# Optimization experiments

Hardware: AMD Instinct MI355X
Metric: run time of the kernel (lower is better)

The kernel has to match this reference:

```python
import jax, jax.numpy as jnp
import numpy as np

N_NODES = 50000
D_MODEL = 128
N_EDGES = 600000
HIDDEN = 128
EDGE_FEAT = 2 * D_MODEL + 2  # 258


def setup_inputs() -> dict:
    key = jax.random.key(0)
    k = jax.random.split(key, 8)
    H = jax.random.normal(k[0], (N_NODES, D_MODEL), dtype=jnp.float32)
    edge_index = jax.random.randint(k[1], (2, N_EDGES), 0, N_NODES, dtype=jnp.int64)
    S_e = jax.random.uniform(k[2], (N_EDGES,), dtype=jnp.float32)
    F_e = jax.random.uniform(k[3], (N_EDGES,), dtype=jnp.float32)
    W1 = jax.random.normal(k[4], (EDGE_FEAT, HIDDEN), dtype=jnp.float32) * (1.0 / np.sqrt(EDGE_FEAT))
    b1 = jnp.zeros((HIDDEN,), dtype=jnp.float32)
    W2 = jax.random.normal(k[5], (HIDDEN, 1), dtype=jnp.float32) * (1.0 / np.sqrt(HIDDEN))
    b2 = jnp.zeros((1,), dtype=jnp.float32)
    return {"H": H, "edge_index": edge_index, "S_e": S_e, "F_e": F_e,
            "W1": W1, "b1": b1, "W2": W2, "b2": b2}


def reference(H, edge_index, S_e, F_e, W1, b1, W2, b2):
    # Gather endpoint node features: [E, D]
    H_u = H[edge_index[0]]
    H_v = H[edge_index[1]]
    H_diff = jnp.abs(H_u - H_v)
    H_prod = H_u * H_v
    # [E, 2D+2]
    edge_features = jnp.concatenate(
        [H_diff, H_prod, S_e[:, None], F_e[:, None]], axis=1)
    # 2-layer MLP with SiLU (dropout is identity in eval mode)
    h = jax.nn.silu(edge_features @ W1 + b1)
    a_e = (h @ W2 + b2)[:, 0]  # [E]
    return a_e
```

## Files before the change

### kernel.cpp

```cpp
#include <hip/hip_runtime.h>


typedef _Float16       half8   __attribute__((ext_vector_type(8)));
typedef _Float16       half4v  __attribute__((ext_vector_type(4)));
typedef unsigned short ushort8 __attribute__((ext_vector_type(8)));
typedef float          f32x4   __attribute__((ext_vector_type(4)));

#define NSEG       8
#define W1T_STRIDE 288

__device__ __forceinline__ float silu_f(float x) {
    return x / (1.0f + __expf(-x));
}

__device__ __forceinline__ void canon(int u, int v, int& a, int& b) {
    const int sw = (u ^ v) & 1;
    a = sw ? v : u;
    b = sw ? u : v;
}


__global__ __launch_bounds__(256)
void cvt_hist_kernel(const float* __restrict__ H, _Float16* __restrict__ Hh,
                     int n4, const int* __restrict__ eidx,
                     int* __restrict__ hist, int E, int ASZ, int BBINS) {
    int i = blockIdx.x * blockDim.x + threadIdx.x;
    if (i < n4) {
        const float4 f = ((const float4*)H)[i];
        half4v h;
        h[0] = (_Float16)f.x; h[1] = (_Float16)f.y;
        h[2] = (_Float16)f.z; h[3] = (_Float16)f.w;
        ((half4v*)Hh)[i] = h;
    }
    if (i < E) {
        int a, b;
        canon(eidx[i], eidx[E + i], a, b);
        atomicAdd(&hist[(a / ASZ) * BBINS + (b >> 3)], 1);
    }
}

__global__ __launch_bounds__(256)
void scan_kernel(int* __restrict__ hist, int* __restrict__ bsum,
                 int NB, int nb1, int* __restrict__ flag,
                 int* __restrict__ vbs, int BBINS, int E) {
    __shared__ int s[256];
    __shared__ int lastBlk;
    const int t = threadIdx.x;
    const int i = blockIdx.x * 256 + t;
    const int v = (i < NB) ? hist[i] : 0;
    s[t] = v;
    __syncthreads();
    for (int off = 1; off < 256; off <<= 1) {
        const int x = (t >= off) ? s[t - off] : 0;
        __syncthreads();
        s[t] += x;
        __syncthreads();
    }
    if (i < NB) hist[i] = s[t] - v;
    if (t == 255) bsum[blockIdx.x] = s[255];
    __threadfence();
    if (t == 0) lastBlk = (atomicAdd(flag, 1) == (int)gridDim.x - 1);
    __syncthreads();
    if (!lastBlk) return;
    const int bv = (t < nb1) ? atomicAdd(&bsum[t], 0) : 0;
    s[t] = bv;
    __syncthreads();
    for (int off = 1; off < 256; off <<= 1) {
        const int x = (t >= off) ? s[t - off] : 0;
        __syncthreads();
        s[t] += x;
        __syncthreads();
    }
    if (t < nb1) bsum[t] = s[t] - bv;
    __syncthreads();
    if (t < NSEG) {
        const int idx = t * BBINS;
        vbs[t] = atomicAdd(&hist[idx], 0) + bsum[idx >> 8];
    } else if (t == NSEG) {
        vbs[NSEG] = E;
    }
}

__global__ __launch_bounds__(256)
void scatter_kernel(const int* __restrict__ eidx, const float* __restrict__ Se,
                    const float* __restrict__ Fe, int* __restrict__ ofs,
                    const int* __restrict__ bsum,
                    int4* __restrict__ recs, int E, int ASZ, int BBINS) {
    int e = blockIdx.x * blockDim.x + threadIdx.x;
    if (e < E) {
        int a, b;
        canon(eidx[e], eidx[E + e], a, b);
        const int key = (a / ASZ) * BBINS + (b >> 3);
        const int pos = atomicAdd(&ofs[key], 1) + bsum[key >> 8];
        _Float16 sh = (_Float16)Se[e];
        _Float16 fh = (_Float16)Fe[e];
        unsigned pk = (unsigned)*(unsigned short*)&sh
                    | ((unsigned)*(unsigned short*)&fh << 16);
        recs[pos] = make_int4(a, b, e, (int)pk);
    }
}


__device__ __forceinline__ void stage_w1(const float* __restrict__ W1,
                                         const float* __restrict__ b1,
                                         _Float16* __restrict__ w1t, int tid) {
    const int n = tid & 127;
    const int g = tid >> 7;
    #pragma unroll
    for (int i = 0; i < 9; ++i) {
        const int kb = g + (i << 2);
        half8 tmp;
        if (kb < 32) {
            #pragma unroll
            for (int j = 0; j < 8; ++j) {
                const int kp  = (kb << 3) + j;
                const int c   = kp >> 5;
                const int k32 = kp & 31;
                const int src = ((c & 1) << 7) + ((c >> 1) << 5) + k32;
                tmp[j] = (_Float16)W1[src * 128 + n];
            }
            *(half8*)&w1t[n * W1T_STRIDE + ((kb ^ (n & 7)) << 3)] = tmp;
        } else {
            const int k32b = (kb - 32) << 3;
            #pragma unroll
            for (int j = 0; j < 8; ++j) {
                const int k32 = k32b + j;
                float v = 0.f;
                if (k32 == 0)      v = W1[32768 + n];
                else if (k32 == 1) v = W1[32896 + n];
                else if (k32 == 2) v = b1[n];
                tmp[j] = (_Float16)v;
            }
            *(half8*)&w1t[n * W1T_STRIDE + (kb << 3)] = tmp;
        }
    }
}


__device__ __forceinline__ void edge_tile32(
    const _Float16* __restrict__ Hh, const int4* __restrict__ recs,
    const _Float16* __restrict__ w1t,
    const f32x4* __restrict__ w2r, float b2v, float* __restrict__ out,
    int ebase, int elim, int q, int cb, int swz)
{
    const int eA = min(ebase + cb, elim - 1);
    const int eB = min(ebase + 16 + cb, elim - 1);
    const int4 rA = recs[eA];
    const int4 rB = recs[eB];

    const _Float16* upA = Hh + (size_t)rA.x * 128;
    const _Float16* vpA = Hh + (size_t)rA.y * 128;
    const _Float16* upB = Hh + (size_t)rB.x * 128;
    const _Float16* vpB = Hh + (size_t)rB.y * 128;

    f32x4 accA[8], accB[8];
    #pragma unroll
    for (int t = 0; t < 8; ++t) {
        accA[t] = (f32x4){0.f, 0.f, 0.f, 0.f};
        accB[t] = (f32x4){0.f, 0.f, 0.f, 0.f};
    }

    #pragma unroll
    for (int c8 = 0; c8 < 4; ++c8) {
        const half8 u8A = *(const half8*)(upA + (c8 << 5) + (q << 3));
        const half8 v8A = *(const half8*)(vpA + (c8 << 5) + (q << 3));
        const half8 u8B = *(const half8*)(upB + (c8 << 5) + (q << 3));
        const half8 v8B = *(const half8*)(vpB + (c8 << 5) + (q << 3));
        half8 dA = u8A - v8A;
        half8 dB = u8B - v8B;
        ushort8 duA = *(ushort8*)&dA; duA = duA & (unsigned short)0x7FFF;
        ushort8 duB = *(ushort8*)&dB; duB = duB & (unsigned short)0x7FFF;
        const half8 aeA = *(half8*)&duA;
        const half8 aeB = *(half8*)&duB;
        const half8 aoA = u8A * v8A;
        const half8 aoB = u8B * v8B;

        const int kb0 = ((c8 << 3) + q) ^ swz;
        const int kb1 = ((c8 << 3) + 4 + q) ^ swz;
        #pragma unroll
        for (int t = 0; t < 8; ++t) {
            const half8 b0 = *(const half8*)&w1t[((t << 4) + cb) * W1T_STRIDE + (kb0 << 3)];
            accA[t] = __builtin_amdgcn_mfma_f32_16x16x32_f16(b0, aeA, accA[t], 0, 0, 0);
            accB[t] = __builtin_amdgcn_mfma_f32_16x16x32_f16(b0, aeB, accB[t], 0, 0, 0);
        }
        #pragma unroll
        for (int t = 0; t < 8; ++t) {
            const half8 b1f = *(const half8*)&w1t[((t << 4) + cb) * W1T_STRIDE + (kb1 << 3)];
            accA[t] = __builtin_amdgcn_mfma_f32_16x16x32_f16(b1f, aoA, accA[t], 0, 0, 0);
            accB[t] = __builtin_amdgcn_mfma_f32_16x16x32_f16(b1f, aoB, accB[t], 0, 0, 0);
        }
    }

    half8 aEA, aEB;
    #pragma unroll
    for (int j = 0; j < 8; ++j) { aEA[j] = (_Float16)0.f; aEB[j] = (_Float16)0.f; }
    if (q == 0) {
        const unsigned short slA = (unsigned short)((unsigned)rA.w & 0xFFFF);
        const unsigned short flA = (unsigned short)((unsigned)rA.w >> 16);
        const unsigned short slB = (unsigned short)((unsigned)rB.w & 0xFFFF);
        const unsigned short flB = (unsigned short)((unsigned)rB.w >> 16);
        aEA[0] = *(const _Float16*)&slA;
        aEA[1] = *(const _Float16*)&flA;
        aEA[2] = (_Float16)1.0f;
        aEB[0] = *(const _Float16*)&slB;
        aEB[1] = *(const _Float16*)&flB;
        aEB[2] = (_Float16)1.0f;
    }
    #pragma unroll
    for (int t = 0; t < 8; ++t) {
        const half8 bE = *(const half8*)&w1t[((t << 4) + cb) * W1T_STRIDE + ((32 + q) << 3)];
        accA[t] = __builtin_amdgcn_mfma_f32_16x16x32_f16(bE, aEA, accA[t], 0, 0, 0);
        accB[t] = __builtin_amdgcn_mfma_f32_16x16x32_f16(bE, aEB, accB[t], 0, 0, 0);
    }

    float rsA = 0.f, rsB = 0.f;
    #pragma unroll
    for (int t = 0; t < 8; ++t) {
        const f32x4 avA = accA[t];
        const f32x4 avB = accB[t];
        const f32x4 wv  = w2r[t];
        #pragma unroll
        for (int rr = 0; rr < 4; ++rr) {
            rsA += silu_f(avA[rr]) * wv[rr];
            rsB += silu_f(avB[rr]) * wv[rr];
        }
    }
    rsA += __shfl_xor(rsA, 16);
    rsA += __shfl_xor(rsA, 32);
    rsB += __shfl_xor(rsB, 16);
    rsB += __shfl_xor(rsB, 32);

    if (q == 0) {
        if (ebase + cb < elim)      out[rA.z] = rsA + b2v;
        if (ebase + 16 + cb < elim) out[rB.z] = rsB + b2v;
    }
}


__global__ __launch_bounds__(512, 2)
void edgegate_seg(const _Float16* __restrict__ Hh,
                  const int4*  __restrict__ recs,
                  const int*   __restrict__ vbs,
                  int*         __restrict__ ctr,
                  const float* __restrict__ W1,
                  const float* __restrict__ b1,
                  const float* __restrict__ W2,
                  const float* __restrict__ b2,
                  float*       __restrict__ out)
{
    __shared__ _Float16 w1t[128 * W1T_STRIDE];
    __shared__ int tkt[2];
    const int tid = threadIdx.x;
    stage_w1(W1, b1, w1t, tid);

    int xcd;
    asm volatile("s_getreg_b32 %0, hwreg(HW_REG_XCC_ID)" : "=s"(xcd));
    xcd &= (NSEG - 1);

    const int lane = tid & 63;
    const int wave = tid >> 6;
    const int q    = lane >> 4;
    const int cb   = lane & 15;
    const int swz  = cb & 7;
    const float b2v = b2[0];
    f32x4 w2r[8];
    #pragma unroll
    for (int t = 0; t < 8; ++t)
        w2r[t] = *(const f32x4*)&W2[(t << 4) + (q << 2)];

    int p = 0;
    for (int sidx = 0; sidx < NSEG; ++sidx) {
        const int seg = (xcd + sidx) & (NSEG - 1);
        const int vs  = vbs[seg];
        const int ve  = vbs[seg + 1];
        const int ner = ve - vs;
        if (ner <= 0) continue;
        const int Tt = (ner + 255) >> 8;

        __syncthreads();
        if (tid == 0) tkt[p] = atomicAdd(&ctr[seg], 1);
        __syncthreads();
        int t0 = tkt[p];
        while (t0 < Tt) {
            const int pn = p ^ 1;
            if (tid == 0) tkt[pn] = atomicAdd(&ctr[seg], 1);
            const int ebase = vs + (t0 << 8) + (wave << 5);
            edge_tile32(Hh, recs, w1t, w2r, b2v, out, ebase, ve, q, cb, swz);
            __syncthreads();
            p = pn;
            t0 = tkt[p];
        }
    }
}


__global__ __launch_bounds__(512, 2)
void edgegate_fb(const float* __restrict__ H,
                 const _Float16* __restrict__ Hh,
                 const int*   __restrict__ eidx,
                 const float* __restrict__ Se,
                 const float* __restrict__ Fe,
                 const float* __restrict__ W1,
                 const float* __restrict__ b1,
                 const float* __restrict__ W2,
                 const float* __restrict__ b2,
                 float*       __restrict__ out,
                 int E, int ntiles, int useF16)
{
    __shared__ _Float16 w1t[128 * W1T_STRIDE];
    const int tid = threadIdx.x;
    stage_w1(W1, b1, w1t, tid);

    const int lane = tid & 63;
    const int wave = tid >> 6;
    const int q    = lane >> 4;
    const int cb   = lane & 15;
    const int swz  = cb & 7;
    const float b2v = b2[0];
    f32x4 w2r[8];
    #pragma unroll
    for (int t = 0; t < 8; ++t)
        w2r[t] = *(const f32x4*)&W2[(t << 4) + (q << 2)];

    __syncthreads();

    for (int tile = blockIdx.x; tile < ntiles; tile += gridDim.x) {
        const int ebase = tile * 128 + wave * 16;
        int e = ebase + cb;
        if (e >= E) e = E - 1;
        const int u = eidx[e];
        const int v = eidx[E + e];
        const float sfe = Se[e];
        const float ffe = Fe[e];

        f32x4 acc[8];
        #pragma unroll
        for (int t = 0; t < 8; ++t) acc[t] = (f32x4){0.f, 0.f, 0.f, 0.f};

        #pragma unroll
        for (int c8 = 0; c8 < 4; ++c8) {
            half8 ae, ao;
            if (useF16) {
                const _Float16* up = Hh + (size_t)u * 128;
                const _Float16* vp = Hh + (size_t)v * 128;
                const half8 u8 = *(const half8*)(up + (c8 << 5) + (q << 3));
                const half8 v8 = *(const half8*)(vp + (c8 << 5) + (q << 3));
                half8 d8 = u8 - v8;
                ushort8 du = *(ushort8*)&d8;
                du = du & (unsigned short)0x7FFF;
                ae = *(half8*)&du;
                ao = u8 * v8;
            } else {
                const float* up = H + (size_t)u * 128;
                const float* vp = H + (size_t)v * 128;
                #pragma unroll
                for (int j = 0; j < 8; ++j) {
                    const float uu = up[(c8 << 5) + (q << 3) + j];
                    const float vv = vp[(c8 << 5) + (q << 3) + j];
                    ae[j] = (_Float16)fabsf(uu - vv);
                    ao[j] = (_Float16)(uu * vv);
                }
            }
            const int kb0 = ((c8 << 3) + q) ^ swz;
            const int kb1 = ((c8 << 3) + 4 + q) ^ swz;
            #pragma unroll
            for (int t = 0; t < 8; ++t) {
                const half8 b0 = *(const half8*)&w1t[((t << 4) + cb) * W1T_STRIDE + (kb0 << 3)];
                acc[t] = __builtin_amdgcn_mfma_f32_16x16x32_f16(b0, ae, acc[t], 0, 0, 0);
            }
            #pragma unroll
            for (int t = 0; t < 8; ++t) {
                const half8 b1f = *(const half8*)&w1t[((t << 4) + cb) * W1T_STRIDE + (kb1 << 3)];
                acc[t] = __builtin_amdgcn_mfma_f32_16x16x32_f16(b1f, ao, acc[t], 0, 0, 0);
            }
        }

        half8 aE;
        #pragma unroll
        for (int j = 0; j < 8; ++j) aE[j] = (_Float16)0.f;
        if (q == 0) {
            aE[0] = (_Float16)sfe;
            aE[1] = (_Float16)ffe;
            aE[2] = (_Float16)1.0f;
        }
        #pragma unroll
        for (int t = 0; t < 8; ++t) {
            const half8 bE = *(const half8*)&w1t[((t << 4) + cb) * W1T_STRIDE + ((32 + q) << 3)];
            acc[t] = __builtin_amdgcn_mfma_f32_16x16x32_f16(bE, aE, acc[t], 0, 0, 0);
        }

        float rs = 0.f;
        #pragma unroll
        for (int t = 0; t < 8; ++t) {
            const f32x4 av = acc[t];
            const f32x4 wv = w2r[t];
            #pragma unroll
            for (int rr = 0; rr < 4; ++rr)
                rs += silu_f(av[rr]) * wv[rr];
        }
        rs += __shfl_xor(rs, 16);
        rs += __shfl_xor(rs, 32);

        if (q == 0 && ebase + cb < E) out[ebase + cb] = rs + b2v;
    }
}


static inline size_t align256(size_t x) { return (x + 255) & ~(size_t)255; }

extern "C" void kernel_launch(void* const* d_in, const int* in_sizes, int n_in,
                              void* d_out, int out_size, void* d_ws, size_t ws_size,
                              hipStream_t stream)
{
    const float* H    = (const float*)d_in[0];
    const int*   eidx = (const int*)  d_in[1];
    const float* Se   = (const float*)d_in[2];
    const float* Fe   = (const float*)d_in[3];
    const float* W1   = (const float*)d_in[4];
    const float* b1   = (const float*)d_in[5];
    const float* W2   = (const float*)d_in[6];
    const float* b2   = (const float*)d_in[7];
    float* out = (float*)d_out;

    const int nH     = in_sizes[0];
    const int nNodes = nH / 128;
    const int E      = in_sizes[2];
    const int n4     = nH / 4;
    const int ntiles = (E + 127) / 128;

    const int ASZ   = (nNodes + NSEG - 1) / NSEG;
    const int BBINS = (nNodes + 7) >> 3;
    const int NB    = NSEG * BBINS;
    const int nb1   = (NB + 255) / 256;

    const size_t hhB    = (size_t)nH * sizeof(_Float16);
    const size_t off_g  = align256(hhB);
    const size_t off_bs = align256(off_g + (size_t)(NB + 16) * 4);
    const size_t off_vb = align256(off_bs + 256 * 4);
    const size_t off_r  = align256(off_vb + 16 * 4);
    const size_t need   = off_r + (size_t)E * sizeof(int4);

    if (ws_size >= need && nb1 <= 256) {
        _Float16* Hh   = (_Float16*)((char*)d_ws);
        int*      hist = (int*)     ((char*)d_ws + off_g);
        int*      ctr  = hist + NB;
        int*      flag = hist + NB + 8;
        int*      bsum = (int*)     ((char*)d_ws + off_bs);
        int*      vbs  = (int*)     ((char*)d_ws + off_vb);
        int4*     recs = (int4*)    ((char*)d_ws + off_r);

        const int ncvh = (n4 > E) ? n4 : E;
        hipMemsetAsync(hist, 0, (size_t)(NB + 16) * sizeof(int), stream);
        hipLaunchKernelGGL(cvt_hist_kernel, dim3((ncvh + 255) / 256), dim3(256),
                           0, stream, H, Hh, n4, eidx, hist, E, ASZ, BBINS);
        hipLaunchKernelGGL(scan_kernel, dim3(nb1), dim3(256), 0, stream,
                           hist, bsum, NB, nb1, flag, vbs, BBINS, E);
        hipLaunchKernelGGL(scatter_kernel, dim3((E + 255) / 256), dim3(256),
                           0, stream, eidx, Se, Fe, hist, bsum, recs,
                           E, ASZ, BBINS);
        hipLaunchKernelGGL(edgegate_seg, dim3(512), dim3(512), 0, stream,
                           Hh, recs, vbs, ctr, W1, b1, W2, b2, out);
    } else if (ws_size >= hhB) {
        _Float16* Hh = (_Float16*)d_ws;
        const int grid = (512 < ntiles) ? 512 : ntiles;
        hipLaunchKernelGGL(cvt_hist_kernel, dim3((n4 + 255) / 256), dim3(256),
                           0, stream, H, Hh, n4, eidx, (int*)nullptr, 0, 1, 1);
        hipLaunchKernelGGL(edgegate_fb, dim3(grid), dim3(512), 0, stream,
                           H, Hh, eidx, Se, Fe, W1, b1, W2, b2, out, E, ntiles, 1);
    } else {
        const int grid = (512 < ntiles) ? 512 : ntiles;
        hipLaunchKernelGGL(edgegate_fb, dim3(grid), dim3(512), 0, stream,
                           H, (const _Float16*)nullptr, eidx, Se, Fe, W1, b1, W2, b2,
                           out, E, ntiles, 0);
    }
}
```

Measured before the change: 299.3 us.

## Split hidden dimension across wave pairs to halve per-wave accumulators

Each tile of 32 edges is now handled by a pair of waves, and each wave computes half of the 128 hidden units, so it holds 4 accumulator tiles per edge group instead of 8. A block now processes 128 edges per ticket instead of 256. Partial second-layer sums are exchanged through shared memory, using a double-buffered slot indexed by the ticket parity, and combined after the existing barrier. The aim is to cut register pressure and per-wave latency, possibly raising occupancy. In exchange, every edge's node features are gathered twice (once per wave of the pair), twice as many tickets are taken, and an extra shared-memory combine is added.

Measured after the change: 305.7 us. 2.1% more time.

```diff
diff --git a/kernel.cpp b/kernel.cpp
--- a/kernel.cpp
+++ b/kernel.cpp
@@ -137,106 +137,6 @@
 }
 
 
-__device__ __forceinline__ void edge_tile32(
-    const _Float16* __restrict__ Hh, const int4* __restrict__ recs,
-    const _Float16* __restrict__ w1t,
-    const f32x4* __restrict__ w2r, float b2v, float* __restrict__ out,
-    int ebase, int elim, int q, int cb, int swz)
-{
-    const int eA = min(ebase + cb, elim - 1);
-    const int eB = min(ebase + 16 + cb, elim - 1);
-    const int4 rA = recs[eA];
-    const int4 rB = recs[eB];
-
-    const _Float16* upA = Hh + (size_t)rA.x * 128;
-    const _Float16* vpA = Hh + (size_t)rA.y * 128;
-    const _Float16* upB = Hh + (size_t)rB.x * 128;
-    const _Float16* vpB = Hh + (size_t)rB.y * 128;
-
-    f32x4 accA[8], accB[8];
-    #pragma unroll
-    for (int t = 0; t < 8; ++t) {
-        accA[t] = (f32x4){0.f, 0.f, 0.f, 0.f};
-        accB[t] = (f32x4){0.f, 0.f, 0.f, 0.f};
-    }
-
-    #pragma unroll
-    for (int c8 = 0; c8 < 4; ++c8) {
-        const half8 u8A = *(const half8*)(upA + (c8 << 5) + (q << 3));
-        const half8 v8A = *(const half8*)(vpA + (c8 << 5) + (q << 3));
-        const half8 u8B = *(const half8*)(upB + (c8 << 5) + (q << 3));
-        const half8 v8B = *(const half8*)(vpB + (c8 << 5) + (q << 3));
-        half8 dA = u8A - v8A;
-        half8 dB = u8B - v8B;
-        ushort8 duA = *(ushort8*)&dA; duA = duA & (unsigned short)0x7FFF;
-        ushort8 duB = *(ushort8*)&dB; duB = duB & (unsigned short)0x7FFF;
-        const half8 aeA = *(half8*)&duA;
-        const half8 aeB = *(half8*)&duB;
-        const half8 aoA = u8A * v8A;
-        const half8 aoB = u8B * v8B;
-
-        const int kb0 = ((c8 << 3) + q) ^ swz;
-        const int kb1 = ((c8 << 3) + 4 + q) ^ swz;
-        #pragma unroll
-        for (int t = 0; t < 8; ++t) {
-            const half8 b0 = *(const half8*)&w1t[((t << 4) + cb) * W1T_STRIDE + (kb0 << 3)];
-            accA[t] = __builtin_amdgcn_mfma_f32_16x16x32_f16(b0, aeA, accA[t], 0, 0, 0);
-            accB[t] = __builtin_amdgcn_mfma_f32_16x16x32_f16(b0, aeB, accB[t], 0, 0, 0);
-        }
-        #pragma unroll
-        for (int t = 0; t < 8; ++t) {
-            const half8 b1f = *(const half8*)&w1t[((t << 4) + cb) * W1T_STRIDE + (kb1 << 3)];
-            accA[t] = __builtin_amdgcn_mfma_f32_16x16x32_f16(b1f, aoA, accA[t], 0, 0, 0);
-            accB[t] = __builtin_amdgcn_mfma_f32_16x16x32_f16(b1f, aoB, accB[t], 0, 0, 0);
-        }
-    }
-
-    half8 aEA, aEB;
-    #pragma unroll
-    for (int j = 0; j < 8; ++j) { aEA[j] = (_Float16)0.f; aEB[j] = (_Float16)0.f; }
-    if (q == 0) {
-        const unsigned short slA = (unsigned short)((unsigned)rA.w & 0xFFFF);
-        const unsigned short flA = (unsigned short)((unsigned)rA.w >> 16);
-        const unsigned short slB = (unsigned short)((unsigned)rB.w & 0xFFFF);
-        const unsigned short flB = (unsigned short)((unsigned)rB.w >> 16);
-        aEA[0] = *(const _Float16*)&slA;
-        aEA[1] = *(const _Float16*)&flA;
-        aEA[2] = (_Float16)1.0f;
-        aEB[0] = *(const _Float16*)&slB;
-        aEB[1] = *(const _Float16*)&flB;
-        aEB[2] = (_Float16)1.0f;
-    }
-    #pragma unroll
-    for (int t = 0; t < 8; ++t) {
-        const half8 bE = *(const half8*)&w1t[((t << 4) + cb) * W1T_STRIDE + ((32 + q) << 3)];
-        accA[t] = __builtin_amdgcn_mfma_f32_16x16x32_f16(bE, aEA, accA[t], 0, 0, 0);
-        accB[t] = __builtin_amdgcn_mfma_f32_16x16x32_f16(bE, aEB, accB[t], 0, 0, 0);
-    }
-
-    float rsA = 0.f, rsB = 0.f;
-    #pragma unroll
-    for (int t = 0; t < 8; ++t) {
-        const f32x4 avA = accA[t];
-        const f32x4 avB = accB[t];
-        const f32x4 wv  = w2r[t];
-        #pragma unroll
-        for (int rr = 0; rr < 4; ++rr) {
-            rsA += silu_f(avA[rr]) * wv[rr];
-            rsB += silu_f(avB[rr]) * wv[rr];
-        }
-    }
-    rsA += __shfl_xor(rsA, 16);
-    rsA += __shfl_xor(rsA, 32);
-    rsB += __shfl_xor(rsB, 16);
-    rsB += __shfl_xor(rsB, 32);
-
-    if (q == 0) {
-        if (ebase + cb < elim)      out[rA.z] = rsA + b2v;
-        if (ebase + 16 + cb < elim) out[rB.z] = rsB + b2v;
-    }
-}
-
-
 __global__ __launch_bounds__(512, 2)
 void edgegate_seg(const _Float16* __restrict__ Hh,
                   const int4*  __restrict__ recs,
@@ -249,6 +149,7 @@
                   float*       __restrict__ out)
 {
     __shared__ _Float16 w1t[128 * W1T_STRIDE];
+    __shared__ float pcomb[2][4][2][16];
     __shared__ int tkt[2];
     const int tid = threadIdx.x;
     stage_w1(W1, b1, w1t, tid);
@@ -259,14 +160,16 @@
 
     const int lane = tid & 63;
     const int wave = tid >> 6;
+    const int pr   = wave >> 1;
+    const int h    = wave & 1;
     const int q    = lane >> 4;
     const int cb   = lane & 15;
     const int swz  = cb & 7;
     const float b2v = b2[0];
-    f32x4 w2r[8];
+    f32x4 w2r[4];
     #pragma unroll
-    for (int t = 0; t < 8; ++t)
-        w2r[t] = *(const f32x4*)&W2[(t << 4) + (q << 2)];
+    for (int tt = 0; tt < 4; ++tt)
+        w2r[tt] = *(const f32x4*)&W2[(((h << 2) + tt) << 4) + (q << 2)];
 
     int p = 0;
     for (int sidx = 0; sidx < NSEG; ++sidx) {
@@ -275,7 +178,7 @@
         const int ve  = vbs[seg + 1];
         const int ner = ve - vs;
         if (ner <= 0) continue;
-        const int Tt = (ner + 255) >> 8;
+        const int Tt = (ner + 127) >> 7;
 
         __syncthreads();
         if (tid == 0) tkt[p] = atomicAdd(&ctr[seg], 1);
@@ -284,9 +187,109 @@
         while (t0 < Tt) {
             const int pn = p ^ 1;
             if (tid == 0) tkt[pn] = atomicAdd(&ctr[seg], 1);
-            const int ebase = vs + (t0 << 8) + (wave << 5);
-            edge_tile32(Hh, recs, w1t, w2r, b2v, out, ebase, ve, q, cb, swz);
+
+            const int ebase = vs + (t0 << 7) + (pr << 5);
+            const int eA = min(ebase + cb, ve - 1);
+            const int eB = min(ebase + 16 + cb, ve - 1);
+            const int4 rA = recs[eA];
+            const int4 rB = recs[eB];
+
+            const _Float16* upA = Hh + (size_t)rA.x * 128;
+            const _Float16* vpA = Hh + (size_t)rA.y * 128;
+            const _Float16* upB = Hh + (size_t)rB.x * 128;
+            const _Float16* vpB = Hh + (size_t)rB.y * 128;
+
+            f32x4 accA[4], accB[4];
+            #pragma unroll
+            for (int tt = 0; tt < 4; ++tt) {
+                accA[tt] = (f32x4){0.f, 0.f, 0.f, 0.f};
+                accB[tt] = (f32x4){0.f, 0.f, 0.f, 0.f};
+            }
+
+            #pragma unroll
+            for (int c8 = 0; c8 < 4; ++c8) {
+                const half8 u8A = *(const half8*)(upA + (c8 << 5) + (q << 3));
+                const half8 v8A = *(const half8*)(vpA + (c8 << 5) + (q << 3));
+                const half8 u8B = *(const half8*)(upB + (c8 << 5) + (q << 3));
+                const half8 v8B = *(const half8*)(vpB + (c8 << 5) + (q << 3));
+                half8 dA = u8A - v8A;
+                half8 dB = u8B - v8B;
+                ushort8 duA = *(ushort8*)&dA; duA = duA & (unsigned short)0x7FFF;
+                ushort8 duB = *(ushort8*)&dB; duB = duB & (unsigned short)0x7FFF;
+                const half8 aeA = *(half8*)&duA;
+                const half8 aeB = *(half8*)&duB;
+                const half8 aoA = u8A * v8A;
+                const half8 aoB = u8B * v8B;
+
+                const int kb0 = ((c8 << 3) + q) ^ swz;
+                const int kb1 = ((c8 << 3) + 4 + q) ^ swz;
+                #pragma unroll
+                for (int tt = 0; tt < 4; ++tt) {
+                    const int row = (((h << 2) + tt) << 4) + cb;
+                    const half8 b0 = *(const half8*)&w1t[row * W1T_STRIDE + (kb0 << 3)];
+                    accA[tt] = __builtin_amdgcn_mfma_f32_16x16x32_f16(b0, aeA, accA[tt], 0, 0, 0);
+                    accB[tt] = __builtin_amdgcn_mfma_f32_16x16x32_f16(b0, aeB, accB[tt], 0, 0, 0);
+                }
+                #pragma unroll
+                for (int tt = 0; tt < 4; ++tt) {
+                    const int row = (((h << 2) + tt) << 4) + cb;
+                    const half8 b1f = *(const half8*)&w1t[row * W1T_STRIDE + (kb1 << 3)];
+                    accA[tt] = __builtin_amdgcn_mfma_f32_16x16x32_f16(b1f, aoA, accA[tt], 0, 0, 0);
+                    accB[tt] = __builtin_amdgcn_mfma_f32_16x16x32_f16(b1f, aoB, accB[tt], 0, 0, 0);
+                }
+            }
+
+            half8 aEA, aEB;
+            #pragma unroll
+            for (int j = 0; j < 8; ++j) { aEA[j] = (_Float16)0.f; aEB[j] = (_Float16)0.f; }
+            if (q == 0) {
+                const unsigned short slA = (unsigned short)((unsigned)rA.w & 0xFFFF);
+                const unsigned short flA = (unsigned short)((unsigned)rA.w >> 16);
+                const unsigned short slB = (unsigned short)((unsigned)rB.w & 0xFFFF);
+                const unsigned short flB = (unsigned short)((unsigned)rB.w >> 16);
+                aEA[0] = *(const _Float16*)&slA;
+                aEA[1] = *(const _Float16*)&flA;
+                aEA[2] = (_Float16)1.0f;
+                aEB[0] = *(const _Float16*)&slB;
+                aEB[1] = *(const _Float16*)&flB;
+                aEB[2] = (_Float16)1.0f;
+            }
+            #pragma unroll
+            for (int tt = 0; tt < 4; ++tt) {
+                const int row = (((h << 2) + tt) << 4) + cb;
+                const half8 bE = *(const half8*)&w1t[row * W1T_STRIDE + ((32 + q) << 3)];
+                accA[tt] = __builtin_amdgcn_mfma_f32_16x16x32_f16(bE, aEA, accA[tt], 0, 0, 0);
+                accB[tt] = __builtin_amdgcn_mfma_f32_16x16x32_f16(bE, aEB, accB[tt], 0, 0, 0);
+            }
+
+            float rsA = 0.f, rsB = 0.f;
+            #pragma unroll
+            for (int tt = 0; tt < 4; ++tt) {
+                const f32x4 avA = accA[tt];
+                const f32x4 avB = accB[tt];
+                const f32x4 wv  = w2r[tt];
+                #pragma unroll
+                for (int rr = 0; rr < 4; ++rr) {
+                    rsA += silu_f(avA[rr]) * wv[rr];
+                    rsB += silu_f(avB[rr]) * wv[rr];
+                }
+            }
+            rsA += __shfl_xor(rsA, 16);
+            rsA += __shfl_xor(rsA, 32);
+            rsB += __shfl_xor(rsB, 16);
+            rsB += __shfl_xor(rsB, 32);
+
+            if (h == 1 && q == 0) {
+                pcomb[p][pr][0][cb] = rsA;
+                pcomb[p][pr][1][cb] = rsB;
+            }
             __syncthreads();
+            if (h == 0 && q == 0) {
+                const float fA = rsA + pcomb[p][pr][0][cb];
+                const float fB = rsB + pcomb[p][pr][1][cb];
+                if (ebase + cb < ve)      out[rA.z] = fA + b2v;
+                if (ebase + 16 + cb < ve) out[rB.z] = fB + b2v;
+            }
             p = pn;
             t0 = tkt[p];
         }
```
